# Optimization experiments

Hardware: AMD Instinct MI355X
Metric: run time of the kernel (lower is better)

The kernel has to match this reference:

```python
import jax, jax.numpy as jnp
import numpy as np


def setup_inputs() -> dict:
    key = jax.random.key(0)
    k1, k2 = jax.random.split(key)
    decoder_hidden = jax.random.normal(k1, (32, 512, 512), dtype=jnp.float32)
    encoder_outputs = jax.random.normal(k2, (32, 2048, 512), dtype=jnp.float32)
    return {"decoder_hidden": decoder_hidden, "encoder_outputs": encoder_outputs}


def reference(decoder_hidden, encoder_outputs):
    # scores: [B, Tq, Tk] = decoder_hidden @ encoder_outputs^T (no 1/sqrt(d) scaling)
    scores = jnp.einsum('bqd,bkd->bqk', decoder_hidden, encoder_outputs)
    attn = jax.nn.softmax(scores, axis=-1)
    # context: [B, Tq, D]
    return jnp.einsum('bqk,bkd->bqd', attn, encoder_outputs)
```

## Files before the change

### kernel.cpp

```cpp
#include <hip/hip_runtime.h>


#define BATCH 32
#define TQ 512
#define TK 2048
#define DIM 512
#define MQ 32
#define NK 16
#define NKT (TK / NK)

typedef __attribute__((ext_vector_type(8))) _Float16 half8;
typedef __attribute__((ext_vector_type(2))) _Float16 half2v;
typedef __attribute__((ext_vector_type(4))) float float4v;
typedef __attribute__((ext_vector_type(4))) int int4v;

__device__ __forceinline__ half2v pkrtz(float a, float b) {
  auto r = __builtin_amdgcn_cvt_pkrtz(a, b);
  half2v o;
  o[0] = (_Float16)r[0];
  o[1] = (_Float16)r[1];
  return o;
}

__global__ __launch_bounds__(256, 2)
void attn_flash3(const float* __restrict__ dec, const float* __restrict__ enc,
                 float* __restrict__ out) {
  const int id = blockIdx.x;
  const int b = ((id & 7) << 2) + ((id >> 3) & 3);
  const int q0 = (id >> 5) * MQ;
  const int tid = threadIdx.x;
  const int wave = tid >> 6;
  const int lane = tid & 63;
  const int quad = lane >> 4;
  const int l16 = lane & 15;

  __shared__ __align__(16) _Float16 KfL[16 * 64 * 8];
  __shared__ __align__(16) _Float16 VtL[DIM * NK];
  __shared__ __align__(16) float Sp[4][MQ][20];

  half8 qhi[2][4], qlo[2][4];
#pragma unroll
  for (int mt = 0; mt < 2; ++mt) {
    const float* qrow =
        dec + ((size_t)b * TQ + (q0 + mt * 16 + l16)) * DIM + wave * 128 + quad * 8;
#pragma unroll
    for (int s = 0; s < 4; ++s) {
      float4v v0 = *(const float4v*)(qrow + s * 32);
      float4v v1 = *(const float4v*)(qrow + s * 32 + 4);
#pragma unroll
      for (int j = 0; j < 4; ++j) {
        float f0 = v0[j], f1 = v1[j];
        _Float16 h0 = (_Float16)f0;
        _Float16 h1 = (_Float16)f1;
        qhi[mt][s][j] = h0;
        qhi[mt][s][j + 4] = h1;
        qlo[mt][s][j] = (_Float16)(f0 - (float)h0);
        qlo[mt][s][j + 4] = (_Float16)(f1 - (float)h1);
      }
    }
  }

  float4v acc[2][8];
#pragma unroll
  for (int mt = 0; mt < 2; ++mt)
#pragma unroll
    for (int t = 0; t < 8; ++t) acc[mt][t] = float4v{0.f, 0.f, 0.f, 0.f};

  float m_r = -INFINITY, l_r = 0.0f;

  const float* encb = enc + (size_t)b * TK * DIM;
  const int key = tid & 15;
  const int drow = tid >> 4;
  const int sgb = drow >> 2;
  const int slot = ((drow & 3) << 4) + key;

  float4v pf[8];
  half8 nxt[4];

  {
    const float* kp = encb + (size_t)key * DIM + drow * 8;
#pragma unroll
    for (int i = 0; i < 4; ++i) {
      pf[2 * i] = *(const float4v*)(kp + i * 128);
      pf[2 * i + 1] = *(const float4v*)(kp + i * 128 + 4);
    }
#pragma unroll
    for (int i = 0; i < 4; ++i) {
      half8 h;
#pragma unroll
      for (int j = 0; j < 4; ++j) {
        h[j] = (_Float16)pf[2 * i][j];
        h[j + 4] = (_Float16)pf[2 * i + 1][j];
      }
      *(half8*)&KfL[((sgb + i * 4) * 64 + slot) * 8] = h;
      nxt[i] = h;
    }
  }
  __syncthreads();

  for (int kt = 0; kt < NKT; ++kt) {
    {
      const int k0n = ((kt + 1) & (NKT - 1)) * NK;
      const float* kp = encb + (size_t)(k0n + key) * DIM + drow * 8;
#pragma unroll
      for (int i = 0; i < 4; ++i) {
        pf[2 * i] = *(const float4v*)(kp + i * 128);
        pf[2 * i + 1] = *(const float4v*)(kp + i * 128 + 4);
      }
    }
#pragma unroll
    for (int i = 0; i < 4; ++i) {
      const int dbase = drow * 8 + i * 128;
#pragma unroll
      for (int j = 0; j < 8; ++j) VtL[(dbase + j) * NK + key] = nxt[i][j];
    }
    {
      float4v s0 = float4v{0.f, 0.f, 0.f, 0.f};
      float4v s1 = float4v{0.f, 0.f, 0.f, 0.f};
      __builtin_amdgcn_s_setprio(1);
#pragma unroll
      for (int s = 0; s < 4; ++s) {
        half8 kf = *(const half8*)&KfL[(((wave << 2) + s) * 64 + lane) * 8];
        s0 = __builtin_amdgcn_mfma_f32_16x16x32_f16(qhi[0][s], kf, s0, 0, 0, 0);
        s0 = __builtin_amdgcn_mfma_f32_16x16x32_f16(qlo[0][s], kf, s0, 0, 0, 0);
        s1 = __builtin_amdgcn_mfma_f32_16x16x32_f16(qhi[1][s], kf, s1, 0, 0, 0);
        s1 = __builtin_amdgcn_mfma_f32_16x16x32_f16(qlo[1][s], kf, s1, 0, 0, 0);
      }
      __builtin_amdgcn_s_setprio(0);
#pragma unroll
      for (int r = 0; r < 4; ++r) {
        Sp[wave][(quad << 2) + r][l16] = s0[r];
        Sp[wave][16 + (quad << 2) + r][l16] = s1[r];
      }
    }
    __syncthreads();

    half8 pB0, pB1;
    float al0, al1;
    {
      const int R = ((quad >> 1) << 4) + l16;
      const int kb = (quad & 1) << 3;
      float4v sa = float4v{0.f, 0.f, 0.f, 0.f};
      float4v sb = float4v{0.f, 0.f, 0.f, 0.f};
#pragma unroll
      for (int w = 0; w < 4; ++w) {
        sa += *(const float4v*)&Sp[w][R][kb];
        sb += *(const float4v*)&Sp[w][R][kb + 4];
      }
      float mx = fmaxf(fmaxf(fmaxf(sa[0], sa[1]), fmaxf(sa[2], sa[3])),
                       fmaxf(fmaxf(sb[0], sb[1]), fmaxf(sb[2], sb[3])));
      mx = fmaxf(mx, __shfl_xor(mx, 16));
      const float mnew = fmaxf(m_r, mx);
      const float al = __expf(m_r - mnew);
      float p[8];
      float sum = 0.0f;
#pragma unroll
      for (int c = 0; c < 4; ++c) { p[c] = __expf(sa[c] - mnew); sum += p[c]; }
#pragma unroll
      for (int c = 0; c < 4; ++c) { p[4 + c] = __expf(sb[c] - mnew); sum += p[4 + c]; }
      sum += __shfl_xor(sum, 16);
      m_r = mnew;
      l_r = l_r * al + sum;
      half8 pown;
#pragma unroll
      for (int pr = 0; pr < 4; ++pr) {
        half2v h = pkrtz(p[2 * pr], p[2 * pr + 1]);
        pown[2 * pr] = h[0];
        pown[2 * pr + 1] = h[1];
      }
      int4v pi = __builtin_bit_cast(int4v, pown);
      int4v ps;
#pragma unroll
      for (int j = 0; j < 4; ++j) ps[j] = __shfl_xor(pi[j], 32);
      half8 psw = __builtin_bit_cast(half8, ps);
      half8 hz;
#pragma unroll
      for (int j = 0; j < 8; ++j) hz[j] = (_Float16)0.0f;
      pB0 = (quad < 2) ? pown : hz;
      pB1 = (quad < 2) ? psw : hz;
      const float alsw = __shfl_xor(al, 32);
      al0 = (quad < 2) ? al : alsw;
      al1 = (quad < 2) ? alsw : al;
    }

    {
      half8 hz;
#pragma unroll
      for (int j = 0; j < 8; ++j) hz[j] = (_Float16)0.0f;
      __builtin_amdgcn_s_setprio(1);
#pragma unroll
      for (int t = 0; t < 8; ++t) {
        const int dd = wave * 128 + t * 16 + l16;
        half8 vf = hz;
        if (quad < 2) vf = *(const half8*)&VtL[dd * NK + quad * 8];
        acc[0][t] = acc[0][t] * al0;
        acc[0][t] = __builtin_amdgcn_mfma_f32_16x16x32_f16(vf, pB0, acc[0][t], 0, 0, 0);
        acc[1][t] = acc[1][t] * al1;
        acc[1][t] = __builtin_amdgcn_mfma_f32_16x16x32_f16(vf, pB1, acc[1][t], 0, 0, 0);
      }
      __builtin_amdgcn_s_setprio(0);
    }

#pragma unroll
    for (int i = 0; i < 4; ++i) {
      half8 h;
#pragma unroll
      for (int j = 0; j < 4; ++j) {
        h[j] = (_Float16)pf[2 * i][j];
        h[j + 4] = (_Float16)pf[2 * i + 1][j];
      }
      *(half8*)&KfL[((sgb + i * 4) * 64 + slot) * 8] = h;
      nxt[i] = h;
    }
    __syncthreads();
  }

  const float lsw = __shfl_xor(l_r, 32);
  const float l0 = (quad < 2) ? l_r : lsw;
  const float l1 = (quad < 2) ? lsw : l_r;
  const float linv0 = 1.0f / l0;
  const float linv1 = 1.0f / l1;
#pragma unroll
  for (int mt = 0; mt < 2; ++mt) {
    const float linv = mt ? linv1 : linv0;
    float* orow =
        out + ((size_t)b * TQ + (q0 + mt * 16 + l16)) * DIM + wave * 128 + quad * 4;
#pragma unroll
    for (int t = 0; t < 8; ++t) {
      float4v o = acc[mt][t] * linv;
      *(float4v*)(orow + t * 16) = o;
    }
  }
}

extern "C" void kernel_launch(void* const* d_in, const int* in_sizes, int n_in,
                              void* d_out, int out_size, void* d_ws, size_t ws_size,
                              hipStream_t stream) {
  const float* dec = (const float*)d_in[0];
  const float* enc = (const float*)d_in[1];
  float* out = (float*)d_out;
  attn_flash3<<<dim3(BATCH * (TQ / MQ)), 256, 0, stream>>>(dec, enc, out);
}
```

Measured before the change: 439.8 us.

## Halve query tile to 16 rows, raise occupancy, add lazy softmax rescaling

Shrinks each block's query tile from 32 to 16 rows. This doubles the grid and raises launch bounds to 4 blocks per CU, and each block keeps a single accumulator set instead of two. Rows are no longer split across quads, so the P fragment is rebuilt with a shuffle network. It also skips rescaling the accumulator unless the new max exceeds the running max by 8 (lazy rescale), which removes the per-tile multiply. The cost is that each encoder tile is now loaded and converted twice as often in total, since K/V reuse per block halves, so global and LDS traffic grow.

```diff
diff --git a/kernel.cpp b/kernel.cpp
--- a/kernel.cpp
+++ b/kernel.cpp
@@ -5,14 +5,14 @@
 #define TQ 512
 #define TK 2048
 #define DIM 512
-#define MQ 32
+#define MQ 16
 #define NK 16
 #define NKT (TK / NK)
 
 typedef __attribute__((ext_vector_type(8))) _Float16 half8;
 typedef __attribute__((ext_vector_type(2))) _Float16 half2v;
 typedef __attribute__((ext_vector_type(4))) float float4v;
-typedef __attribute__((ext_vector_type(4))) int int4v;
+typedef __attribute__((ext_vector_type(4))) unsigned int uint4v;
 
 __device__ __forceinline__ half2v pkrtz(float a, float b) {
   auto r = __builtin_amdgcn_cvt_pkrtz(a, b);
@@ -22,8 +22,13 @@
   return o;
 }
 
-__global__ __launch_bounds__(256, 2)
-void attn_flash3(const float* __restrict__ dec, const float* __restrict__ enc,
+__device__ __forceinline__ unsigned int pkrtz_u32(float a, float b) {
+  half2v h = pkrtz(a, b);
+  return __builtin_bit_cast(unsigned int, h);
+}
+
+__global__ __launch_bounds__(256, 4)
+void attn_flash6(const float* __restrict__ dec, const float* __restrict__ enc,
                  float* __restrict__ out) {
   const int id = blockIdx.x;
   const int b = ((id & 7) << 2) + ((id >> 3) & 3);
@@ -38,11 +43,10 @@
   __shared__ __align__(16) _Float16 VtL[DIM * NK];
   __shared__ __align__(16) float Sp[4][MQ][20];
 
-  half8 qhi[2][4], qlo[2][4];
-#pragma unroll
-  for (int mt = 0; mt < 2; ++mt) {
+  half8 qhi[4], qlo[4];
+  {
     const float* qrow =
-        dec + ((size_t)b * TQ + (q0 + mt * 16 + l16)) * DIM + wave * 128 + quad * 8;
+        dec + ((size_t)b * TQ + (q0 + l16)) * DIM + wave * 128 + quad * 8;
 #pragma unroll
     for (int s = 0; s < 4; ++s) {
       float4v v0 = *(const float4v*)(qrow + s * 32);
@@ -52,19 +56,17 @@
         float f0 = v0[j], f1 = v1[j];
         _Float16 h0 = (_Float16)f0;
         _Float16 h1 = (_Float16)f1;
-        qhi[mt][s][j] = h0;
-        qhi[mt][s][j + 4] = h1;
-        qlo[mt][s][j] = (_Float16)(f0 - (float)h0);
-        qlo[mt][s][j + 4] = (_Float16)(f1 - (float)h1);
-      }
-    }
-  }
-
-  float4v acc[2][8];
-#pragma unroll
-  for (int mt = 0; mt < 2; ++mt)
-#pragma unroll
-    for (int t = 0; t < 8; ++t) acc[mt][t] = float4v{0.f, 0.f, 0.f, 0.f};
+        qhi[s][j] = h0;
+        qhi[s][j + 4] = h1;
+        qlo[s][j] = (_Float16)(f0 - (float)h0);
+        qlo[s][j + 4] = (_Float16)(f1 - (float)h1);
+      }
+    }
+  }
+
+  float4v acc[8];
+#pragma unroll
+  for (int t = 0; t < 8; ++t) acc[t] = float4v{0.f, 0.f, 0.f, 0.f};
 
   float m_r = -INFINITY, l_r = 0.0f;
 
@@ -116,71 +118,72 @@
     }
     {
       float4v s0 = float4v{0.f, 0.f, 0.f, 0.f};
-      float4v s1 = float4v{0.f, 0.f, 0.f, 0.f};
       __builtin_amdgcn_s_setprio(1);
 #pragma unroll
       for (int s = 0; s < 4; ++s) {
         half8 kf = *(const half8*)&KfL[(((wave << 2) + s) * 64 + lane) * 8];
-        s0 = __builtin_amdgcn_mfma_f32_16x16x32_f16(qhi[0][s], kf, s0, 0, 0, 0);
-        s0 = __builtin_amdgcn_mfma_f32_16x16x32_f16(qlo[0][s], kf, s0, 0, 0, 0);
-        s1 = __builtin_amdgcn_mfma_f32_16x16x32_f16(qhi[1][s], kf, s1, 0, 0, 0);
-        s1 = __builtin_amdgcn_mfma_f32_16x16x32_f16(qlo[1][s], kf, s1, 0, 0, 0);
+        s0 = __builtin_amdgcn_mfma_f32_16x16x32_f16(qhi[s], kf, s0, 0, 0, 0);
+        s0 = __builtin_amdgcn_mfma_f32_16x16x32_f16(qlo[s], kf, s0, 0, 0, 0);
       }
       __builtin_amdgcn_s_setprio(0);
 #pragma unroll
       for (int r = 0; r < 4; ++r) {
         Sp[wave][(quad << 2) + r][l16] = s0[r];
-        Sp[wave][16 + (quad << 2) + r][l16] = s1[r];
       }
     }
     __syncthreads();
 
-    half8 pB0, pB1;
-    float al0, al1;
-    {
-      const int R = ((quad >> 1) << 4) + l16;
-      const int kb = (quad & 1) << 3;
+    half8 pB;
+    {
+      const int kb = quad << 2;
       float4v sa = float4v{0.f, 0.f, 0.f, 0.f};
-      float4v sb = float4v{0.f, 0.f, 0.f, 0.f};
 #pragma unroll
       for (int w = 0; w < 4; ++w) {
-        sa += *(const float4v*)&Sp[w][R][kb];
-        sb += *(const float4v*)&Sp[w][R][kb + 4];
-      }
-      float mx = fmaxf(fmaxf(fmaxf(sa[0], sa[1]), fmaxf(sa[2], sa[3])),
-                       fmaxf(fmaxf(sb[0], sb[1]), fmaxf(sb[2], sb[3])));
+        sa += *(const float4v*)&Sp[w][l16][kb];
+      }
+      float mx = fmaxf(fmaxf(sa[0], sa[1]), fmaxf(sa[2], sa[3]));
       mx = fmaxf(mx, __shfl_xor(mx, 16));
-      const float mnew = fmaxf(m_r, mx);
-      const float al = __expf(m_r - mnew);
-      float p[8];
+      mx = fmaxf(mx, __shfl_xor(mx, 32));
+      if (!__all(mx <= m_r + 8.0f)) {
+        const float mnew = fmaxf(m_r, mx);
+        const float al = __expf(m_r - mnew);
+        m_r = mnew;
+        l_r *= al;
+#pragma unroll
+        for (int t = 0; t < 8; ++t) acc[t] *= al;
+      }
+      float p[4];
       float sum = 0.0f;
 #pragma unroll
-      for (int c = 0; c < 4; ++c) { p[c] = __expf(sa[c] - mnew); sum += p[c]; }
-#pragma unroll
-      for (int c = 0; c < 4; ++c) { p[4 + c] = __expf(sb[c] - mnew); sum += p[4 + c]; }
+      for (int c = 0; c < 4; ++c) {
+        p[c] = __expf(sa[c] - m_r);
+        sum += p[c];
+      }
       sum += __shfl_xor(sum, 16);
-      m_r = mnew;
-      l_r = l_r * al + sum;
-      half8 pown;
-#pragma unroll
-      for (int pr = 0; pr < 4; ++pr) {
-        half2v h = pkrtz(p[2 * pr], p[2 * pr + 1]);
-        pown[2 * pr] = h[0];
-        pown[2 * pr + 1] = h[1];
-      }
-      int4v pi = __builtin_bit_cast(int4v, pown);
-      int4v ps;
-#pragma unroll
-      for (int j = 0; j < 4; ++j) ps[j] = __shfl_xor(pi[j], 32);
-      half8 psw = __builtin_bit_cast(half8, ps);
-      half8 hz;
-#pragma unroll
-      for (int j = 0; j < 8; ++j) hz[j] = (_Float16)0.0f;
-      pB0 = (quad < 2) ? pown : hz;
-      pB1 = (quad < 2) ? psw : hz;
-      const float alsw = __shfl_xor(al, 32);
-      al0 = (quad < 2) ? al : alsw;
-      al1 = (quad < 2) ? alsw : al;
+      sum += __shfl_xor(sum, 32);
+      l_r += sum;
+
+      unsigned int w0 = pkrtz_u32(p[0], p[1]);
+      unsigned int w1 = pkrtz_u32(p[2], p[3]);
+      unsigned int pw0 = __shfl_xor(w0, 16);
+      unsigned int pw1 = __shfl_xor(w1, 16);
+      unsigned int a0 = (quad & 1) ? pw0 : w0;
+      unsigned int a1 = (quad & 1) ? pw1 : w1;
+      unsigned int a2 = (quad & 1) ? w0 : pw0;
+      unsigned int a3 = (quad & 1) ? w1 : pw1;
+      unsigned int b0 = __shfl_xor(a0, 32);
+      unsigned int b1 = __shfl_xor(a1, 32);
+      unsigned int b2 = __shfl_xor(a2, 32);
+      unsigned int b3 = __shfl_xor(a3, 32);
+      uint4v pw;
+      if (quad == 0) {
+        pw = uint4v{a0, a1, a2, a3};
+      } else if (quad == 1) {
+        pw = uint4v{b0, b1, b2, b3};
+      } else {
+        pw = uint4v{0u, 0u, 0u, 0u};
+      }
+      pB = __builtin_bit_cast(half8, pw);
     }
 
     {
@@ -193,10 +196,7 @@
         const int dd = wave * 128 + t * 16 + l16;
         half8 vf = hz;
         if (quad < 2) vf = *(const half8*)&VtL[dd * NK + quad * 8];
-        acc[0][t] = acc[0][t] * al0;
-        acc[0][t] = __builtin_amdgcn_mfma_f32_16x16x32_f16(vf, pB0, acc[0][t], 0, 0, 0);
-        acc[1][t] = acc[1][t] * al1;
-        acc[1][t] = __builtin_amdgcn_mfma_f32_16x16x32_f16(vf, pB1, acc[1][t], 0, 0, 0);
+        acc[t] = __builtin_amdgcn_mfma_f32_16x16x32_f16(vf, pB, acc[t], 0, 0, 0);
       }
       __builtin_amdgcn_s_setprio(0);
     }
@@ -215,21 +215,13 @@
     __syncthreads();
   }
 
-  const float lsw = __shfl_xor(l_r, 32);
-  const float l0 = (quad < 2) ? l_r : lsw;
-  const float l1 = (quad < 2) ? lsw : l_r;
-  const float linv0 = 1.0f / l0;
-  const float linv1 = 1.0f / l1;
-#pragma unroll
-  for (int mt = 0; mt < 2; ++mt) {
-    const float linv = mt ? linv1 : linv0;
-    float* orow =
-        out + ((size_t)b * TQ + (q0 + mt * 16 + l16)) * DIM + wave * 128 + quad * 4;
-#pragma unroll
-    for (int t = 0; t < 8; ++t) {
-      float4v o = acc[mt][t] * linv;
-      *(float4v*)(orow + t * 16) = o;
-    }
+  const float linv = 1.0f / l_r;
+  float* orow =
+      out + ((size_t)b * TQ + (q0 + l16)) * DIM + wave * 128 + quad * 4;
+#pragma unroll
+  for (int t = 0; t < 8; ++t) {
+    float4v o = acc[t] * linv;
+    *(float4v*)(orow + t * 16) = o;
   }
 }
 
@@ -239,5 +231,5 @@
   const float* dec = (const float*)d_in[0];
   const float* enc = (const float*)d_in[1];
   float* out = (float*)d_out;
-  attn_flash3<<<dim3(BATCH * (TQ / MQ)), 256, 0, stream>>>(dec, enc, out);
-}
+  attn_flash6<<<dim3(BATCH * (TQ / MQ)), 256, 0, stream>>>(dec, enc, out);
+}
```

Result: slower. 694.7 us (+58.0%).

## Use 16x16x16 MFMA for PV, lazy rescale with threshold, padded V stride

Applied to the files above, without the earlier changes.

The PV product now uses the 16x16x16 f16 MFMA with half4 operands instead of a 16x16x32 MFMA whose upper half was zero-padded, which removes the wasted half of the matrix work. The softmax reduction is restructured so each lane holds both query tiles, with max and sum reduced across four quads. Accumulator rescaling is skipped unless the running max grows by more than 8, which cuts the multiplies per tile. The V tile in LDS gets a padded stride of 20 to reduce bank conflicts. The lazy rescale can let unnormalised values grow by up to e^8, which stays safe in fp16 P only because the threshold is small.

```diff
diff --git a/kernel.cpp b/kernel.cpp
--- a/kernel.cpp
+++ b/kernel.cpp
@@ -8,11 +8,12 @@
 #define MQ 32
 #define NK 16
 #define NKT (TK / NK)
+#define VSTR 20
 
 typedef __attribute__((ext_vector_type(8))) _Float16 half8;
+typedef __attribute__((ext_vector_type(4))) _Float16 half4;
 typedef __attribute__((ext_vector_type(2))) _Float16 half2v;
 typedef __attribute__((ext_vector_type(4))) float float4v;
-typedef __attribute__((ext_vector_type(4))) int int4v;
 
 __device__ __forceinline__ half2v pkrtz(float a, float b) {
   auto r = __builtin_amdgcn_cvt_pkrtz(a, b);
@@ -23,7 +24,7 @@
 }
 
 __global__ __launch_bounds__(256, 2)
-void attn_flash3(const float* __restrict__ dec, const float* __restrict__ enc,
+void attn_flash8(const float* __restrict__ dec, const float* __restrict__ enc,
                  float* __restrict__ out) {
   const int id = blockIdx.x;
   const int b = ((id & 7) << 2) + ((id >> 3) & 3);
@@ -35,7 +36,7 @@
   const int l16 = lane & 15;
 
   __shared__ __align__(16) _Float16 KfL[16 * 64 * 8];
-  __shared__ __align__(16) _Float16 VtL[DIM * NK];
+  __shared__ __align__(16) _Float16 VtL[DIM * VSTR];
   __shared__ __align__(16) float Sp[4][MQ][20];
 
   half8 qhi[2][4], qlo[2][4];
@@ -66,7 +67,8 @@
 #pragma unroll
     for (int t = 0; t < 8; ++t) acc[mt][t] = float4v{0.f, 0.f, 0.f, 0.f};
 
-  float m_r = -INFINITY, l_r = 0.0f;
+  float m0 = -INFINITY, l0 = 0.0f;
+  float m1 = -INFINITY, l1 = 0.0f;
 
   const float* encb = enc + (size_t)b * TK * DIM;
   const int key = tid & 15;
@@ -112,7 +114,7 @@
     for (int i = 0; i < 4; ++i) {
       const int dbase = drow * 8 + i * 128;
 #pragma unroll
-      for (int j = 0; j < 8; ++j) VtL[(dbase + j) * NK + key] = nxt[i][j];
+      for (int j = 0; j < 8; ++j) VtL[(dbase + j) * VSTR + key] = nxt[i][j];
     }
     {
       float4v s0 = float4v{0.f, 0.f, 0.f, 0.f};
@@ -135,68 +137,66 @@
     }
     __syncthreads();
 
-    half8 pB0, pB1;
-    float al0, al1;
-    {
-      const int R = ((quad >> 1) << 4) + l16;
-      const int kb = (quad & 1) << 3;
+    half4 pB0, pB1;
+    {
+      const int kb = quad << 2;
       float4v sa = float4v{0.f, 0.f, 0.f, 0.f};
       float4v sb = float4v{0.f, 0.f, 0.f, 0.f};
 #pragma unroll
       for (int w = 0; w < 4; ++w) {
-        sa += *(const float4v*)&Sp[w][R][kb];
-        sb += *(const float4v*)&Sp[w][R][kb + 4];
-      }
-      float mx = fmaxf(fmaxf(fmaxf(sa[0], sa[1]), fmaxf(sa[2], sa[3])),
-                       fmaxf(fmaxf(sb[0], sb[1]), fmaxf(sb[2], sb[3])));
-      mx = fmaxf(mx, __shfl_xor(mx, 16));
-      const float mnew = fmaxf(m_r, mx);
-      const float al = __expf(m_r - mnew);
-      float p[8];
-      float sum = 0.0f;
-#pragma unroll
-      for (int c = 0; c < 4; ++c) { p[c] = __expf(sa[c] - mnew); sum += p[c]; }
-#pragma unroll
-      for (int c = 0; c < 4; ++c) { p[4 + c] = __expf(sb[c] - mnew); sum += p[4 + c]; }
-      sum += __shfl_xor(sum, 16);
-      m_r = mnew;
-      l_r = l_r * al + sum;
-      half8 pown;
-#pragma unroll
-      for (int pr = 0; pr < 4; ++pr) {
-        half2v h = pkrtz(p[2 * pr], p[2 * pr + 1]);
-        pown[2 * pr] = h[0];
-        pown[2 * pr + 1] = h[1];
-      }
-      int4v pi = __builtin_bit_cast(int4v, pown);
-      int4v ps;
-#pragma unroll
-      for (int j = 0; j < 4; ++j) ps[j] = __shfl_xor(pi[j], 32);
-      half8 psw = __builtin_bit_cast(half8, ps);
-      half8 hz;
-#pragma unroll
-      for (int j = 0; j < 8; ++j) hz[j] = (_Float16)0.0f;
-      pB0 = (quad < 2) ? pown : hz;
-      pB1 = (quad < 2) ? psw : hz;
-      const float alsw = __shfl_xor(al, 32);
-      al0 = (quad < 2) ? al : alsw;
-      al1 = (quad < 2) ? alsw : al;
-    }
-
-    {
-      half8 hz;
-#pragma unroll
-      for (int j = 0; j < 8; ++j) hz[j] = (_Float16)0.0f;
+        sa += *(const float4v*)&Sp[w][l16][kb];
+        sb += *(const float4v*)&Sp[w][16 + l16][kb];
+      }
+      float mx0 = fmaxf(fmaxf(sa[0], sa[1]), fmaxf(sa[2], sa[3]));
+      float mx1 = fmaxf(fmaxf(sb[0], sb[1]), fmaxf(sb[2], sb[3]));
+      mx0 = fmaxf(mx0, __shfl_xor(mx0, 16));
+      mx0 = fmaxf(mx0, __shfl_xor(mx0, 32));
+      mx1 = fmaxf(mx1, __shfl_xor(mx1, 16));
+      mx1 = fmaxf(mx1, __shfl_xor(mx1, 32));
+      if (!__all(mx0 <= m0 + 8.0f && mx1 <= m1 + 8.0f)) {
+        const float mn0 = fmaxf(m0, mx0);
+        const float mn1 = fmaxf(m1, mx1);
+        const float al0 = __expf(m0 - mn0);
+        const float al1 = __expf(m1 - mn1);
+        m0 = mn0; m1 = mn1;
+        l0 *= al0; l1 *= al1;
+#pragma unroll
+        for (int t = 0; t < 8; ++t) {
+          acc[0][t] *= al0;
+          acc[1][t] *= al1;
+        }
+      }
+      float p0[4], p1[4];
+      float s0 = 0.0f, s1 = 0.0f;
+#pragma unroll
+      for (int c = 0; c < 4; ++c) {
+        p0[c] = __expf(sa[c] - m0);
+        s0 += p0[c];
+        p1[c] = __expf(sb[c] - m1);
+        s1 += p1[c];
+      }
+      s0 += __shfl_xor(s0, 16);
+      s0 += __shfl_xor(s0, 32);
+      s1 += __shfl_xor(s1, 16);
+      s1 += __shfl_xor(s1, 32);
+      l0 += s0;
+      l1 += s1;
+      half2v a0 = pkrtz(p0[0], p0[1]);
+      half2v a1 = pkrtz(p0[2], p0[3]);
+      half2v b0v = pkrtz(p1[0], p1[1]);
+      half2v b1v = pkrtz(p1[2], p1[3]);
+      pB0[0] = a0[0]; pB0[1] = a0[1]; pB0[2] = a1[0]; pB0[3] = a1[1];
+      pB1[0] = b0v[0]; pB1[1] = b0v[1]; pB1[2] = b1v[0]; pB1[3] = b1v[1];
+    }
+
+    {
       __builtin_amdgcn_s_setprio(1);
 #pragma unroll
       for (int t = 0; t < 8; ++t) {
         const int dd = wave * 128 + t * 16 + l16;
-        half8 vf = hz;
-        if (quad < 2) vf = *(const half8*)&VtL[dd * NK + quad * 8];
-        acc[0][t] = acc[0][t] * al0;
-        acc[0][t] = __builtin_amdgcn_mfma_f32_16x16x32_f16(vf, pB0, acc[0][t], 0, 0, 0);
-        acc[1][t] = acc[1][t] * al1;
-        acc[1][t] = __builtin_amdgcn_mfma_f32_16x16x32_f16(vf, pB1, acc[1][t], 0, 0, 0);
+        half4 vf = *(const half4*)&VtL[dd * VSTR + (quad << 2)];
+        acc[0][t] = __builtin_amdgcn_mfma_f32_16x16x16f16(vf, pB0, acc[0][t], 0, 0, 0);
+        acc[1][t] = __builtin_amdgcn_mfma_f32_16x16x16f16(vf, pB1, acc[1][t], 0, 0, 0);
       }
       __builtin_amdgcn_s_setprio(0);
     }
@@ -215,16 +215,13 @@
     __syncthreads();
   }
 
-  const float lsw = __shfl_xor(l_r, 32);
-  const float l0 = (quad < 2) ? l_r : lsw;
-  const float l1 = (quad < 2) ? lsw : l_r;
   const float linv0 = 1.0f / l0;
   const float linv1 = 1.0f / l1;
 #pragma unroll
   for (int mt = 0; mt < 2; ++mt) {
     const float linv = mt ? linv1 : linv0;
     float* orow =
-        out + ((size_t)b * TQ + (q0 + mt * 16 + l16)) * DIM + wave * 128 + quad * 4;
+        out + ((size_t)b * TQ + (q0 + mt * 16 + l16)) * DIM + wave * 128 + (quad << 2);
 #pragma unroll
     for (int t = 0; t < 8; ++t) {
       float4v o = acc[mt][t] * linv;
@@ -239,5 +236,5 @@
   const float* dec = (const float*)d_in[0];
   const float* enc = (const float*)d_in[1];
   float* out = (float*)d_out;
-  attn_flash3<<<dim3(BATCH * (TQ / MQ)), 256, 0, stream>>>(dec, enc, out);
+  attn_flash8<<<dim3(BATCH * (TQ / MQ)), 256, 0, stream>>>(dec, enc, out);
 }
```

Result: faster. 418.8 us (-4.8%).
